# Kernel tuning notes

Hardware: AMD Instinct MI355X
Metric: run time of the kernel (lower is better)

## Reference

```python
import jax, jax.numpy as jnp
import numpy as np

N_NODES = 50000
N_EDGES = 800000
H_DIM = 128
N_REL = 40
N_BASES = 4


def setup_inputs() -> dict:
    key = jax.random.key(0)
    ks = jax.random.split(key, 9)
    h = jax.random.normal(ks[0], (N_NODES, H_DIM), jnp.float32)
    norm = jax.random.uniform(ks[1], (N_EDGES, 1), jnp.float32)
    basis_w = jax.random.normal(ks[2], (N_BASES, H_DIM, H_DIM), jnp.float32) * 0.05
    w_comp = jax.random.normal(ks[3], (N_REL, N_BASES), jnp.float32) * 0.5
    loop_w = jax.random.normal(ks[4], (H_DIM, H_DIM), jnp.float32) * 0.05
    bias = jax.random.normal(ks[5], (H_DIM,), jnp.float32) * 0.05
    src = jax.random.randint(ks[6], (N_EDGES,), 0, N_NODES, jnp.int32)
    dst = jax.random.randint(ks[7], (N_EDGES,), 0, N_NODES, jnp.int32)
    etype = jax.random.randint(ks[8], (N_EDGES,), 0, N_REL, jnp.int32)
    return {"h": h, "norm": norm, "basis_w": basis_w, "w_comp": w_comp,
            "loop_w": loop_w, "bias": bias, "src": src, "dst": dst, "etype": etype}


def reference(h, norm, basis_w, w_comp, loop_w, bias, src, dst, etype):
    # RelGraphConv with 'basis' regularizer, one layer (num_hidden_layers=1):
    #   W_r = sum_b w_comp[r, b] * basis_w[b]
    #   m_e = (h[src_e] @ W_{etype_e}) * norm_e
    #   agg[v] = sum_{e: dst_e = v} m_e
    #   out = relu(agg + bias + h @ loop_w)   (dropout = 0)
    # Contraction reordered for memory efficiency: scatter-add per-basis
    # scaled source features first (node-level), then apply small basis GEMMs.
    n = h.shape[0]
    n_bases = basis_w.shape[0]
    coeff = w_comp[etype] * norm          # [E, B] per-edge basis coefficients * norm
    h_src = h[src]                        # [E, D] edge-gathered source features
    agg = jnp.zeros((n, basis_w.shape[2]), dtype=h.dtype)
    for b in range(n_bases):              # small fixed loop over bases
        s_b = jax.ops.segment_sum(coeff[:, b:b + 1] * h_src, dst, num_segments=n)  # [N, D]
        agg = agg + s_b @ basis_w[b]
    return jax.nn.relu(agg + bias + h @ loop_w)
```

## Files before the change

### kernel.cpp

```cpp
#include <hip/hip_runtime.h>
#include <stdint.h>

#define N_NODES 50000
#define N_EDGES 800000
#define H_DIM 128
#define N_REL 40
#define N_BASES 4
#define N_RANGES 196
#define EP_BLOCKS 400
#define EDGES_PER_BLK 2000
#define STAGE_CAP 5120
#define CAST_BLOCKS 1563

typedef __attribute__((ext_vector_type(8))) short bf16x8;
typedef __attribute__((ext_vector_type(4))) float f32x4;

__device__ __forceinline__ unsigned short f2bf(float f) {
    unsigned int u = __float_as_uint(f);
    unsigned int r = u + 0x7fffu + ((u >> 16) & 1u);
    return (unsigned short)(r >> 16);
}

__global__ __launch_bounds__(512) void edge_pack(
        const int* __restrict__ src, const int* __restrict__ dst,
        const int* __restrict__ etype, const float* __restrict__ norm,
        uint2* __restrict__ pkd, int* __restrict__ gcnt,
        unsigned* __restrict__ sorted_src, float4* __restrict__ sorted_cf) {
    __shared__ int lhist[N_RANGES];
    int blk = blockIdx.x;
    int t = threadIdx.x;
    if (t < N_RANGES) lhist[t] = 0;
    if (blk == 0 && t >= 496) {
        int k = t - 496;
        sorted_src[N_EDGES + k] = 0u;
        sorted_cf[N_EDGES + k] = make_float4(0.f, 0.f, 0.f, 0.f);
    }
    __syncthreads();
    int e0 = blk * EDGES_PER_BLK;
    for (int i = t; i < EDGES_PER_BLK; i += 512) {
        int e = e0 + i;
        int d = dst[e];
        unsigned int nbf = f2bf(norm[e]);
        pkd[e] = make_uint2((unsigned)src[e] | ((unsigned)etype[e] << 20),
                            (unsigned)d | (nbf << 17));
        atomicAdd(&lhist[d >> 8], 1);
    }
    __syncthreads();
    if (t < N_RANGES) gcnt[blk * N_RANGES + t] = lhist[t];
}

__global__ __launch_bounds__(512) void stage2(
        const float* __restrict__ h,
        const float* __restrict__ basis_w, const float* __restrict__ loop_w,
        const uint2* __restrict__ pkd, const int* __restrict__ gcnt,
        unsigned short* __restrict__ A, unsigned short* __restrict__ wt3,
        uint2* __restrict__ bucketed) {
    __shared__ int lcur[N_RANGES];
    __shared__ int wsum[8];
    int bid = blockIdx.x;
    int t = threadIdx.x;
    if (bid < EP_BLOCKS) {
        int lane = t & 63, w = t >> 6;
        int b = bid;
        int tot = 0, pre = 0;
        if (t < N_RANGES) {
            for (int bb = 0; bb < EP_BLOCKS; ++bb) {
                int g = gcnt[bb * N_RANGES + t];
                tot += g;
                if (bb < b) pre += g;
            }
        }
        int x = (t < N_RANGES) ? tot : 0;
        int v = x;
#pragma unroll
        for (int d = 1; d < 64; d <<= 1) {
            int y = __shfl_up(v, d);
            if (lane >= d) v += y;
        }
        if (lane == 63) wsum[w] = v;
        __syncthreads();
        int wpre = 0;
#pragma unroll
        for (int ww = 0; ww < 7; ++ww)
            if (w > ww) wpre += wsum[ww];
        if (t < N_RANGES)
            lcur[t] = (wpre + v - x) + pre;
        __syncthreads();
        int e0 = b * EDGES_PER_BLK;
        for (int i = t; i < EDGES_PER_BLK; i += 512) {
            uint2 p = pkd[e0 + i];
            int r = (p.y & 0x1FFFF) >> 8;
            int pos = atomicAdd(&lcur[r], 1);
            bucketed[pos] = p;
        }
    } else if (bid < EP_BLOCKS + CAST_BLOCKS) {
        int g = (bid - EP_BLOCKS) * 512 + t;
        if (g < 800000) {
            int row = g >> 4;
            int cb = (g & 15) * 8;
            const float* p = h + (size_t)row * 128 + cb;
            float4 a0 = ((const float4*)p)[0];
            float4 a1 = ((const float4*)p)[1];
            bf16x8 o;
            o[0] = (short)f2bf(a0.x); o[1] = (short)f2bf(a0.y);
            o[2] = (short)f2bf(a0.z); o[3] = (short)f2bf(a0.w);
            o[4] = (short)f2bf(a1.x); o[5] = (short)f2bf(a1.y);
            o[6] = (short)f2bf(a1.z); o[7] = (short)f2bf(a1.w);
            *(bf16x8*)(A + (size_t)row * H_DIM + cb) = o;
        }
    } else {
        int mat = bid - EP_BLOCKS - CAST_BLOCKS;
        const float* srcm = (mat < 4) ? (basis_w + mat * 16384) : loop_w;
        int koff = (mat < 4) ? (128 + mat * 128) : 0;
#pragma unroll
        for (int i = 0; i < 8; ++i) {
            int f = t + i * 512;
            int k = f >> 5;
            int j4 = (f & 31) * 4;
            float4 v = ((const float4*)srcm)[f];
            int kg = koff + k;
            int ks = kg >> 5;
            int quad = (kg >> 3) & 3;
            int jj = kg & 7;
            float vv[4] = {v.x, v.y, v.z, v.w};
#pragma unroll
            for (int d = 0; d < 4; ++d) {
                int j = j4 + d;
                int cg = j >> 4;
                int n16 = j & 15;
                wt3[(size_t)((ks * 8 + cg) * 64 + quad * 16 + n16) * 8 + jj] =
                    f2bf(vv[d]);
            }
        }
    }
}

__global__ __launch_bounds__(512) void bucket_sort(
        const int* __restrict__ gcnt, const uint2* __restrict__ bucketed,
        const float* __restrict__ w_comp,
        unsigned* __restrict__ sorted_src, float4* __restrict__ sorted_cf,
        int* __restrict__ offs) {
    __shared__ int hist[256];
    __shared__ int cur[256];
    __shared__ int wsum[8];
    __shared__ int sbeg;
    __shared__ int stot;
    __shared__ uint2 stage[STAGE_CAP];
    int r = blockIdx.x;
    int t = threadIdx.x, lane = t & 63, w = t >> 6;
    int tot = 0;
    if (t < N_RANGES)
        for (int bb = 0; bb < EP_BLOCKS; ++bb)
            tot += gcnt[bb * N_RANGES + t];
    int x = (t < N_RANGES) ? tot : 0;
    int v = x;
#pragma unroll
    for (int d = 1; d < 64; d <<= 1) {
        int y = __shfl_up(v, d);
        if (lane >= d) v += y;
    }
    if (lane == 63) wsum[w] = v;
    if (t < 256) hist[t] = 0;
    __syncthreads();
    int wpre = 0;
#pragma unroll
    for (int ww = 0; ww < 7; ++ww)
        if (w > ww) wpre += wsum[ww];
    if (t == r) { sbeg = wpre + v - x; stot = x; }
    __syncthreads();
    int begin = sbeg;
    int end = begin + stot;
    int n = end - begin;
    for (int i = begin + t; i < end; i += 512)
        atomicAdd(&hist[bucketed[i].y & 255], 1);
    __syncthreads();
    int x2 = (t < 256) ? hist[t] : 0;
    int v2 = x2;
#pragma unroll
    for (int d = 1; d < 64; d <<= 1) {
        int y = __shfl_up(v2, d);
        if (lane >= d) v2 += y;
    }
    if (lane == 63) wsum[w] = v2;
    __syncthreads();
    int wpre2 = 0;
#pragma unroll
    for (int ww = 0; ww < 3; ++ww)
        if (w > ww) wpre2 += wsum[ww];
    if (t < 256) {
        int excl_rel = wpre2 + v2 - x2;
        int node = r * 256 + t;
        if (node < N_NODES) offs[node] = begin + excl_rel;
        cur[t] = excl_rel;
    }
    if (r == N_RANGES - 1 && t == 0) offs[N_NODES] = N_EDGES;
    __syncthreads();
    if (n <= STAGE_CAP) {
        for (int i = begin + t; i < end; i += 512) {
            uint2 p = bucketed[i];
            int pos = atomicAdd(&cur[p.y & 255], 1);
            stage[pos] = make_uint2(p.x, (p.y >> 17) << 16);
        }
        __syncthreads();
        for (int i = t; i < n; i += 512) {
            uint2 p = stage[i];
            float nm = __uint_as_float(p.y);
            float4 wc = ((const float4*)w_comp)[p.x >> 20];
            sorted_src[begin + i] = p.x & 0xFFFFF;
            sorted_cf[begin + i] =
                make_float4(wc.x * nm, wc.y * nm, wc.z * nm, wc.w * nm);
        }
    } else {
        for (int i = begin + t; i < end; i += 512) {
            uint2 p = bucketed[i];
            int pos = atomicAdd(&cur[p.y & 255], 1);
            float nm = __uint_as_float((p.y >> 17) << 16);
            float4 wc = ((const float4*)w_comp)[p.x >> 20];
            sorted_src[begin + pos] = p.x & 0xFFFFF;
            sorted_cf[begin + pos] =
                make_float4(wc.x * nm, wc.y * nm, wc.z * nm, wc.w * nm);
        }
    }
}

__global__ __launch_bounds__(512, 8) void agg_gemm(
        const int* __restrict__ offs, const unsigned* __restrict__ ssrc,
        const float4* __restrict__ scf,
        const unsigned short* __restrict__ Ab,
        const unsigned short* __restrict__ wt3,
        const float* __restrict__ bias, float* __restrict__ out) {
    __shared__ __align__(16) unsigned short S[32 * 640];
    int wv = threadIdx.x >> 6;
    int lane = threadIdx.x & 63;
    int nbase = blockIdx.x * 32;
    const unsigned int* Au = (const unsigned int*)Ab;

#pragma unroll
    for (int q = 0; q < 4; ++q) {
        int row = (wv << 2) + q;
        int v = __builtin_amdgcn_readfirstlane(nbase + row);
        float a0l = 0.f, a0h = 0.f, a1l = 0.f, a1h = 0.f;
        float a2l = 0.f, a2h = 0.f, a3l = 0.f, a3h = 0.f;
        unsigned int hb = 0u;
        if (v < N_NODES) {
            hb = Au[(size_t)v * 64 + lane];
            int begin = __builtin_amdgcn_readfirstlane(offs[v]);
            int end   = __builtin_amdgcn_readfirstlane(offs[v + 1]);
            for (int j = begin; j < end; j += 8) {
                int rem = end - j;
                unsigned su[8];
                float4 c[8];
#pragma unroll
                for (int k = 0; k < 8; ++k) su[k] = ssrc[j + k];
#pragma unroll
                for (int k = 0; k < 8; ++k) c[k] = scf[j + k];
                if (rem < 8) {
#pragma unroll
                    for (int k = 0; k < 8; ++k)
                        if (k >= rem) {
                            su[k] = 0u;
                            c[k] = make_float4(0.f, 0.f, 0.f, 0.f);
                        }
                }
                unsigned u[8];
#pragma unroll
                for (int k = 0; k < 8; ++k)
                    u[k] = Au[(size_t)su[k] * 64 + lane];
#pragma unroll
                for (int k = 0; k < 8; ++k) {
                    float lo = __uint_as_float(u[k] << 16);
                    float hi = __uint_as_float(u[k] & 0xffff0000u);
                    a0l += c[k].x * lo; a0h += c[k].x * hi;
                    a1l += c[k].y * lo; a1h += c[k].y * hi;
                    a2l += c[k].z * lo; a2h += c[k].z * hi;
                    a3l += c[k].w * lo; a3h += c[k].w * hi;
                }
            }
        }
        char* rp = (char*)S + row * 1280;
        int swz = (row & 7) << 4;
        *(unsigned int*)(rp + ((lane * 4) ^ swz)) = hb;
        *(unsigned int*)(rp + ((256 + lane * 4) ^ swz)) =
            (unsigned int)f2bf(a0l) | ((unsigned int)f2bf(a0h) << 16);
        *(unsigned int*)(rp + ((512 + lane * 4) ^ swz)) =
            (unsigned int)f2bf(a1l) | ((unsigned int)f2bf(a1h) << 16);
        *(unsigned int*)(rp + ((768 + lane * 4) ^ swz)) =
            (unsigned int)f2bf(a2l) | ((unsigned int)f2bf(a2h) << 16);
        *(unsigned int*)(rp + ((1024 + lane * 4) ^ swz)) =
            (unsigned int)f2bf(a3l) | ((unsigned int)f2bf(a3h) << 16);
    }
    __syncthreads();

    int n16 = lane & 15;
    int quad = lane >> 4;
    f32x4 acc0 = (f32x4)0.f, acc1 = (f32x4)0.f;

    const char* s0p = (const char*)S + n16 * 1280;
    const char* s1p = s0p + 16 * 1280;
    int swz2 = (n16 & 7) << 4;
    const unsigned short* bwp = wt3 + (size_t)wv * 512 + (size_t)lane * 8;

#pragma unroll
    for (int ks = 0; ks < 20; ++ks) {
        int off = (ks * 64 + quad * 16) ^ swz2;
        bf16x8 a0 = *(const bf16x8*)(s0p + off);
        bf16x8 a1 = *(const bf16x8*)(s1p + off);
        bf16x8 b  = *(const bf16x8*)(bwp + (size_t)ks * 4096);
        acc0 = __builtin_amdgcn_mfma_f32_16x16x32_bf16(a0, b, acc0, 0, 0, 0);
        acc1 = __builtin_amdgcn_mfma_f32_16x16x32_bf16(a1, b, acc1, 0, 0, 0);
    }

    int col = (wv << 4) + n16;
    float bv = bias[col];
#pragma unroll
    for (int rg = 0; rg < 4; ++rg) {
        int r0 = nbase + quad * 4 + rg;
        if (r0 < N_NODES)
            out[(size_t)r0 * H_DIM + col] = fmaxf(acc0[rg] + bv, 0.f);
        int r1 = nbase + 16 + quad * 4 + rg;
        if (r1 < N_NODES)
            out[(size_t)r1 * H_DIM + col] = fmaxf(acc1[rg] + bv, 0.f);
    }
}

extern "C" void kernel_launch(void* const* d_in, const int* in_sizes, int n_in,
                              void* d_out, int out_size, void* d_ws, size_t ws_size,
                              hipStream_t stream) {
    const float* h       = (const float*)d_in[0];
    const float* norm    = (const float*)d_in[1];
    const float* basis_w = (const float*)d_in[2];
    const float* w_comp  = (const float*)d_in[3];
    const float* loop_w  = (const float*)d_in[4];
    const float* bias    = (const float*)d_in[5];
    const int*   src     = (const int*)d_in[6];
    const int*   dst     = (const int*)d_in[7];
    const int*   etype   = (const int*)d_in[8];
    float* out = (float*)d_out;

    char* base = (char*)d_ws;
    unsigned short* wt3       = (unsigned short*)(base + 0);
    unsigned short* A         = (unsigned short*)(base + 163840);
    int*            offs      = (int*)(base + 12963840);
    uint2*          pkd       = (uint2*)(base + 13163848);
    uint2*          bucketed  = (uint2*)(base + 19563848);
    float4*         sorted_cf = (float4*)(base + 25963856);
    unsigned*       sorted_src= (unsigned*)(base + 38764112);
    int*            gcnt      = (int*)(base + 41964176);

    edge_pack<<<EP_BLOCKS, 512, 0, stream>>>(src, dst, etype, norm,
                                             pkd, gcnt,
                                             sorted_src, sorted_cf);
    stage2<<<EP_BLOCKS + CAST_BLOCKS + 5, 512, 0, stream>>>(
        h, basis_w, loop_w, pkd, gcnt, A, wt3, bucketed);
    bucket_sort<<<N_RANGES, 512, 0, stream>>>(gcnt, bucketed, w_comp,
                                              sorted_src, sorted_cf, offs);
    agg_gemm<<<1563, 512, 0, stream>>>(offs, sorted_src, sorted_cf,
                                       A, wt3, bias, out);
}
```

Before: 179.2 us.

## Precompute per-range block prefix sums in a separate scan kernel

Adds a bucket_scan_a kernel that computes, for each destination range, the exclusive prefix of per-block counts and the range totals in parallel. stage2 and bucket_sort previously had 196 threads each looping serially over 400 block counts with strided global reads, and they now read the precomputed values directly. edge_pack and bucket_sort are also widened to 1024 threads per block. The cost is one extra kernel launch and more workspace.

```diff
diff --git a/kernel.cpp b/kernel.cpp
--- a/kernel.cpp
+++ b/kernel.cpp
@@ -21,7 +21,7 @@
     return (unsigned short)(r >> 16);
 }
 
-__global__ __launch_bounds__(512) void edge_pack(
+__global__ __launch_bounds__(1024) void edge_pack(
         const int* __restrict__ src, const int* __restrict__ dst,
         const int* __restrict__ etype, const float* __restrict__ norm,
         uint2* __restrict__ pkd, int* __restrict__ gcnt,
@@ -30,14 +30,14 @@
     int blk = blockIdx.x;
     int t = threadIdx.x;
     if (t < N_RANGES) lhist[t] = 0;
-    if (blk == 0 && t >= 496) {
-        int k = t - 496;
+    if (blk == 0 && t >= 1008) {
+        int k = t - 1008;
         sorted_src[N_EDGES + k] = 0u;
         sorted_cf[N_EDGES + k] = make_float4(0.f, 0.f, 0.f, 0.f);
     }
     __syncthreads();
     int e0 = blk * EDGES_PER_BLK;
-    for (int i = t; i < EDGES_PER_BLK; i += 512) {
+    for (int i = t; i < EDGES_PER_BLK; i += 1024) {
         int e = e0 + i;
         int d = dst[e];
         unsigned int nbf = f2bf(norm[e]);
@@ -49,10 +49,34 @@
     if (t < N_RANGES) gcnt[blk * N_RANGES + t] = lhist[t];
 }
 
+__global__ __launch_bounds__(512) void bucket_scan_a(
+        const int* __restrict__ gcnt, int* __restrict__ blkbase,
+        int* __restrict__ btot) {
+    __shared__ int wsum[8];
+    int r = blockIdx.x;
+    int t = threadIdx.x, lane = t & 63, w = t >> 6;
+    int x = (t < EP_BLOCKS) ? gcnt[t * N_RANGES + r] : 0;
+    int v = x;
+#pragma unroll
+    for (int d = 1; d < 64; d <<= 1) {
+        int y = __shfl_up(v, d);
+        if (lane >= d) v += y;
+    }
+    if (lane == 63) wsum[w] = v;
+    __syncthreads();
+    int wpre = 0;
+#pragma unroll
+    for (int ww = 0; ww < 7; ++ww)
+        if (w > ww) wpre += wsum[ww];
+    if (t < EP_BLOCKS) blkbase[t * N_RANGES + r] = wpre + v - x;
+    if (t == 511) btot[r] = wpre + v;
+}
+
 __global__ __launch_bounds__(512) void stage2(
         const float* __restrict__ h,
         const float* __restrict__ basis_w, const float* __restrict__ loop_w,
-        const uint2* __restrict__ pkd, const int* __restrict__ gcnt,
+        const uint2* __restrict__ pkd, const int* __restrict__ blkbase,
+        const int* __restrict__ btot,
         unsigned short* __restrict__ A, unsigned short* __restrict__ wt3,
         uint2* __restrict__ bucketed) {
     __shared__ int lcur[N_RANGES];
@@ -62,15 +86,7 @@
     if (bid < EP_BLOCKS) {
         int lane = t & 63, w = t >> 6;
         int b = bid;
-        int tot = 0, pre = 0;
-        if (t < N_RANGES) {
-            for (int bb = 0; bb < EP_BLOCKS; ++bb) {
-                int g = gcnt[bb * N_RANGES + t];
-                tot += g;
-                if (bb < b) pre += g;
-            }
-        }
-        int x = (t < N_RANGES) ? tot : 0;
+        int x = (t < N_RANGES) ? btot[t] : 0;
         int v = x;
 #pragma unroll
         for (int d = 1; d < 64; d <<= 1) {
@@ -84,7 +100,7 @@
         for (int ww = 0; ww < 7; ++ww)
             if (w > ww) wpre += wsum[ww];
         if (t < N_RANGES)
-            lcur[t] = (wpre + v - x) + pre;
+            lcur[t] = (wpre + v - x) + blkbase[b * N_RANGES + t];
         __syncthreads();
         int e0 = b * EDGES_PER_BLK;
         for (int i = t; i < EDGES_PER_BLK; i += 512) {
@@ -135,24 +151,19 @@
     }
 }
 
-__global__ __launch_bounds__(512) void bucket_sort(
-        const int* __restrict__ gcnt, const uint2* __restrict__ bucketed,
+__global__ __launch_bounds__(1024) void bucket_sort(
+        const int* __restrict__ btot, const uint2* __restrict__ bucketed,
         const float* __restrict__ w_comp,
         unsigned* __restrict__ sorted_src, float4* __restrict__ sorted_cf,
         int* __restrict__ offs) {
     __shared__ int hist[256];
     __shared__ int cur[256];
-    __shared__ int wsum[8];
+    __shared__ int wsum[16];
     __shared__ int sbeg;
-    __shared__ int stot;
     __shared__ uint2 stage[STAGE_CAP];
     int r = blockIdx.x;
     int t = threadIdx.x, lane = t & 63, w = t >> 6;
-    int tot = 0;
-    if (t < N_RANGES)
-        for (int bb = 0; bb < EP_BLOCKS; ++bb)
-            tot += gcnt[bb * N_RANGES + t];
-    int x = (t < N_RANGES) ? tot : 0;
+    int x = (t < N_RANGES) ? btot[t] : 0;
     int v = x;
 #pragma unroll
     for (int d = 1; d < 64; d <<= 1) {
@@ -164,14 +175,14 @@
     __syncthreads();
     int wpre = 0;
 #pragma unroll
-    for (int ww = 0; ww < 7; ++ww)
+    for (int ww = 0; ww < 15; ++ww)
         if (w > ww) wpre += wsum[ww];
-    if (t == r) { sbeg = wpre + v - x; stot = x; }
+    if (t == r) sbeg = wpre + v - x;
     __syncthreads();
     int begin = sbeg;
-    int end = begin + stot;
-    int n = end - begin;
-    for (int i = begin + t; i < end; i += 512)
+    int n = btot[r];
+    int end = begin + n;
+    for (int i = begin + t; i < end; i += 1024)
         atomicAdd(&hist[bucketed[i].y & 255], 1);
     __syncthreads();
     int x2 = (t < 256) ? hist[t] : 0;
@@ -183,11 +194,11 @@
     }
     if (lane == 63) wsum[w] = v2;
     __syncthreads();
-    int wpre2 = 0;
-#pragma unroll
-    for (int ww = 0; ww < 3; ++ww)
-        if (w > ww) wpre2 += wsum[ww];
     if (t < 256) {
+        int wpre2 = 0;
+#pragma unroll
+        for (int ww = 0; ww < 3; ++ww)
+            if (w > ww) wpre2 += wsum[ww];
         int excl_rel = wpre2 + v2 - x2;
         int node = r * 256 + t;
         if (node < N_NODES) offs[node] = begin + excl_rel;
@@ -196,13 +207,13 @@
     if (r == N_RANGES - 1 && t == 0) offs[N_NODES] = N_EDGES;
     __syncthreads();
     if (n <= STAGE_CAP) {
-        for (int i = begin + t; i < end; i += 512) {
+        for (int i = begin + t; i < end; i += 1024) {
             uint2 p = bucketed[i];
             int pos = atomicAdd(&cur[p.y & 255], 1);
             stage[pos] = make_uint2(p.x, (p.y >> 17) << 16);
         }
         __syncthreads();
-        for (int i = t; i < n; i += 512) {
+        for (int i = t; i < n; i += 1024) {
             uint2 p = stage[i];
             float nm = __uint_as_float(p.y);
             float4 wc = ((const float4*)w_comp)[p.x >> 20];
@@ -211,7 +222,7 @@
                 make_float4(wc.x * nm, wc.y * nm, wc.z * nm, wc.w * nm);
         }
     } else {
-        for (int i = begin + t; i < end; i += 512) {
+        for (int i = begin + t; i < end; i += 1024) {
             uint2 p = bucketed[i];
             int pos = atomicAdd(&cur[p.y & 255], 1);
             float nm = __uint_as_float((p.y >> 17) << 16);
@@ -346,14 +357,17 @@
     float4*         sorted_cf = (float4*)(base + 25963856);
     unsigned*       sorted_src= (unsigned*)(base + 38764112);
     int*            gcnt      = (int*)(base + 41964176);
-
-    edge_pack<<<EP_BLOCKS, 512, 0, stream>>>(src, dst, etype, norm,
-                                             pkd, gcnt,
-                                             sorted_src, sorted_cf);
+    int*            blkbase   = (int*)(base + 42277776);
+    int*            btot      = (int*)(base + 42591376);
+
+    edge_pack<<<EP_BLOCKS, 1024, 0, stream>>>(src, dst, etype, norm,
+                                              pkd, gcnt,
+                                              sorted_src, sorted_cf);
+    bucket_scan_a<<<N_RANGES, 512, 0, stream>>>(gcnt, blkbase, btot);
     stage2<<<EP_BLOCKS + CAST_BLOCKS + 5, 512, 0, stream>>>(
-        h, basis_w, loop_w, pkd, gcnt, A, wt3, bucketed);
-    bucket_sort<<<N_RANGES, 512, 0, stream>>>(gcnt, bucketed, w_comp,
-                                              sorted_src, sorted_cf, offs);
+        h, basis_w, loop_w, pkd, blkbase, btot, A, wt3, bucketed);
+    bucket_sort<<<N_RANGES, 1024, 0, stream>>>(btot, bucketed, w_comp,
+                                               sorted_src, sorted_cf, offs);
     agg_gemm<<<1563, 512, 0, stream>>>(offs, sorted_src, sorted_cf,
                                        A, wt3, bias, out);
 }
```

New measurement: 166.5 us, median of 2. 1.08x faster.
